# Kernel optimization log

Measured on AMD Instinct MI355X. Metric: run time of the kernel, lower is better.

The kernel has to match this reference:

```python
import jax, jax.numpy as jnp
import numpy as np

B, N, OUT = 32, 2048, 100

def setup_inputs() -> dict:
    key = jax.random.key(0)
    k1, k2 = jax.random.split(key)
    query = jax.random.normal(k1, (B, N), dtype=jnp.float32) * 10.0
    # Dense(100, use_bias=False) kernel, glorot-ish scale
    W = jax.random.normal(k2, (N, OUT), dtype=jnp.float32) * (1.0 / np.sqrt(N))
    return {"query": query, "W": W}

def reference(query, W):
    # Faithful translation of the TF graph:
    # cast -> expand_dims(1)/(2) -> broadcast add -> cast -> reduce_sum(axis=1)
    c = query.astype(jnp.int32)                      # [B, N]
    g = c[:, None, :] + c[:, :, None]                # [B, N, N], g[b,i,j] = c[b,j] + c[b,i]
    f = g.astype(jnp.float32)
    f_reduced = jnp.sum(f, axis=1)                   # [B, N] == N*c[b,j] + sum_i c[b,i]
    diff = query - f_reduced
    rem = diff * diff                                # squared diff
    return rem @ W                                   # [B, 100]
```

## Files before the change

### kernel.cpp

```cpp
#include <hip/hip_runtime.h>

#define BATCH  32
#define NDIM   2048
#define NOUT   100
#define OG     8
#define NOG    13
#define BLOCK  256
#define NCHUNK (BLOCK / OG)
#define CHUNK  (NDIM / NCHUNK)

__global__ __launch_bounds__(BLOCK)
void fused_model_kernel(const float* __restrict__ q,
                        const float* __restrict__ W,
                        float* __restrict__ out)
{
    const int g = blockIdx.x;
    const int b = blockIdx.y;
    const int t = threadIdx.x;

    __shared__ float rem_lds[NDIM];
    __shared__ int   wave_sum[BLOCK / 64];
    __shared__ float wred[BLOCK / 64][OG];
    __shared__ int   S_lds;

    const float4* qrow4 = (const float4*)(q + b * NDIM);
    const float4 v0 = qrow4[t];
    const float4 v1 = qrow4[BLOCK + t];

    const int c0x = (int)v0.x, c0y = (int)v0.y, c0z = (int)v0.z, c0w = (int)v0.w;
    const int c1x = (int)v1.x, c1y = (int)v1.y, c1z = (int)v1.z, c1w = (int)v1.w;
    int csum = c0x + c0y + c0z + c0w + c1x + c1y + c1z + c1w;

    #pragma unroll
    for (int m = 32; m > 0; m >>= 1) csum += __shfl_xor(csum, m, 64);
    if ((t & 63) == 0) wave_sum[t >> 6] = csum;
    __syncthreads();
    if (t == 0)
        S_lds = wave_sum[0] + wave_sum[1] + wave_sum[2] + wave_sum[3];
    __syncthreads();
    const int S = S_lds;

    {
        const int j0 = 4 * t, j1 = 4 * BLOCK + 4 * t;
        float d;
        d = v0.x - (float)(NDIM * c0x + S); rem_lds[j0 + 0] = d * d;
        d = v0.y - (float)(NDIM * c0y + S); rem_lds[j0 + 1] = d * d;
        d = v0.z - (float)(NDIM * c0z + S); rem_lds[j0 + 2] = d * d;
        d = v0.w - (float)(NDIM * c0w + S); rem_lds[j0 + 3] = d * d;
        d = v1.x - (float)(NDIM * c1x + S); rem_lds[j1 + 0] = d * d;
        d = v1.y - (float)(NDIM * c1y + S); rem_lds[j1 + 1] = d * d;
        d = v1.z - (float)(NDIM * c1z + S); rem_lds[j1 + 2] = d * d;
        d = v1.w - (float)(NDIM * c1w + S); rem_lds[j1 + 3] = d * d;
    }
    __syncthreads();

    const int o    = t & (OG - 1);
    const int ch   = t >> 3;
    const int ocol = g * OG + o;
    const int jb   = ch * CHUNK;

    float acc = 0.f;
    if (ocol < NOUT) {
        const float* Wb = W + (size_t)jb * NOUT + ocol;
        #pragma unroll 8
        for (int j = 0; j < CHUNK; ++j)
            acc += rem_lds[jb + j] * Wb[(size_t)j * NOUT];
    }

    acc += __shfl_xor(acc, 8, 64);
    acc += __shfl_xor(acc, 16, 64);
    acc += __shfl_xor(acc, 32, 64);
    if ((t & 63) < OG) wred[t >> 6][o] = acc;
    __syncthreads();

    if (t < OG) {
        const int oc = g * OG + t;
        if (oc < NOUT)
            out[b * NOUT + oc] = wred[0][t] + wred[1][t] + wred[2][t] + wred[3][t];
    }
}

extern "C" void kernel_launch(void* const* d_in, const int* in_sizes, int n_in,
                              void* d_out, int out_size, void* d_ws, size_t ws_size,
                              hipStream_t stream) {
    const float* q = (const float*)d_in[0];
    const float* W = (const float*)d_in[1];
    float* out = (float*)d_out;

    dim3 grid(NOG, BATCH);
    fused_model_kernel<<<grid, BLOCK, 0, stream>>>(q, W, out);
}
```

Baseline: 59.91 us.

## Vectorize W loads as float4 per thread and shrink reduction chunks

Each thread now handles four adjacent output columns and loads them from W as one float4, so each block splits the 2048-long reduction into 128 chunks of 16 rows instead of 32 chunks of 64. The rem values for a chunk are read from LDS with vector loads into registers, and the reduction shuffles are widened to cover four accumulators. The separate sync that broadcast S through LDS is dropped; every thread now sums the four wave partials itself. The aim is fewer, wider global load instructions and more rows in flight per block, at the cost of more registers and more shuffle work.

```diff
diff --git a/kernel.cpp b/kernel.cpp
--- a/kernel.cpp
+++ b/kernel.cpp
@@ -6,7 +6,7 @@
 #define OG     8
 #define NOG    13
 #define BLOCK  256
-#define NCHUNK (BLOCK / OG)
+#define NCHUNK (BLOCK / 2)
 #define CHUNK  (NDIM / NCHUNK)
 
 __global__ __launch_bounds__(BLOCK)
@@ -18,10 +18,9 @@
     const int b = blockIdx.y;
     const int t = threadIdx.x;
 
-    __shared__ float rem_lds[NDIM];
+    __shared__ __align__(16) float rem_lds[NDIM];
     __shared__ int   wave_sum[BLOCK / 64];
     __shared__ float wred[BLOCK / 64][OG];
-    __shared__ int   S_lds;
 
     const float4* qrow4 = (const float4*)(q + b * NDIM);
     const float4 v0 = qrow4[t];
@@ -35,10 +34,7 @@
     for (int m = 32; m > 0; m >>= 1) csum += __shfl_xor(csum, m, 64);
     if ((t & 63) == 0) wave_sum[t >> 6] = csum;
     __syncthreads();
-    if (t == 0)
-        S_lds = wave_sum[0] + wave_sum[1] + wave_sum[2] + wave_sum[3];
-    __syncthreads();
-    const int S = S_lds;
+    const int S = wave_sum[0] + wave_sum[1] + wave_sum[2] + wave_sum[3];
 
     {
         const int j0 = 4 * t, j1 = 4 * BLOCK + 4 * t;
@@ -54,23 +50,46 @@
     }
     __syncthreads();
 
-    const int o    = t & (OG - 1);
-    const int ch   = t >> 3;
-    const int ocol = g * OG + o;
+    const int o4   = t & 1;
+    const int ch   = t >> 1;
     const int jb   = ch * CHUNK;
+    const int colb = g * OG + 4 * o4;
 
-    float acc = 0.f;
-    if (ocol < NOUT) {
-        const float* Wb = W + (size_t)jb * NOUT + ocol;
-        #pragma unroll 8
-        for (int j = 0; j < CHUNK; ++j)
-            acc += rem_lds[jb + j] * Wb[(size_t)j * NOUT];
+    float ax = 0.f, ay = 0.f, az = 0.f, aw = 0.f;
+    if (colb < NOUT) {
+        const float4* Wp = (const float4*)(W + (size_t)jb * NOUT + colb);
+        const float4* rp = (const float4*)(rem_lds + jb);
+
+        float r[CHUNK];
+        #pragma unroll
+        for (int k = 0; k < CHUNK / 4; ++k) {
+            const float4 rv = rp[k];
+            r[4 * k + 0] = rv.x; r[4 * k + 1] = rv.y;
+            r[4 * k + 2] = rv.z; r[4 * k + 3] = rv.w;
+        }
+        #pragma unroll
+        for (int j = 0; j < CHUNK; ++j) {
+            const float4 wv = Wp[(size_t)j * (NOUT / 4)];
+            ax += r[j] * wv.x;
+            ay += r[j] * wv.y;
+            az += r[j] * wv.z;
+            aw += r[j] * wv.w;
+        }
     }
 
-    acc += __shfl_xor(acc, 8, 64);
-    acc += __shfl_xor(acc, 16, 64);
-    acc += __shfl_xor(acc, 32, 64);
-    if ((t & 63) < OG) wred[t >> 6][o] = acc;
+    #pragma unroll
+    for (int m = 2; m <= 32; m <<= 1) {
+        ax += __shfl_xor(ax, m, 64);
+        ay += __shfl_xor(ay, m, 64);
+        az += __shfl_xor(az, m, 64);
+        aw += __shfl_xor(aw, m, 64);
+    }
+    if ((t & 63) < 2) {
+        float* wr = wred[t >> 6];
+        const int base = 4 * (t & 1);
+        wr[base + 0] = ax; wr[base + 1] = ay;
+        wr[base + 2] = az; wr[base + 3] = aw;
+    }
     __syncthreads();
 
     if (t < OG) {
```

New measurement: 59.86 us. No clear change (-0.1%).
